# Kernel optimization log

Hardware: AMD Instinct MI355X
Metric: run time of the kernel (lower is better)

## Reference

```python
import jax, jax.numpy as jnp
import numpy as np

B, S, NX, NH = 4, 2048, 1024, 16
HD = NX // NH
MASKED_BIAS = -10000.0


def setup_inputs() -> dict:
    key = jax.random.key(0)
    k1, k2, k3 = jax.random.split(key, 3)
    return {
        "hidden_states": jax.random.normal(k1, (B, S, NX), dtype=jnp.float32),
        "c_attn_w": jax.random.normal(k2, (NX, 3 * NX), dtype=jnp.float32) * 0.02,
        "c_attn_b": jnp.zeros((3 * NX,), dtype=jnp.float32),
        "c_proj_w": jax.random.normal(k3, (NX, NX), dtype=jnp.float32) * 0.02,
        "c_proj_b": jnp.zeros((NX,), dtype=jnp.float32),
    }


def reference(hidden_states, c_attn_w, c_attn_b, c_proj_w, c_proj_b):
    b, s, nx = hidden_states.shape
    # fused QKV projection (Conv1D == x @ W + b)
    qkv = hidden_states @ c_attn_w + c_attn_b          # [b, s, 3*nx]
    q, k, v = jnp.split(qkv, 3, axis=-1)
    # split heads -> [b, h, s, d]
    q = q.reshape(b, s, NH, HD).transpose(0, 2, 1, 3)
    k = k.reshape(b, s, NH, HD).transpose(0, 2, 1, 3)
    v = v.reshape(b, s, NH, HD).transpose(0, 2, 1, 3)
    # scaled scores [b, h, s, s]
    w = jnp.einsum("bhqd,bhkd->bhqk", q, k) / jnp.float32(np.sqrt(HD))
    # causal mask via torch.where(mask, w, -10000.0) semantics
    causal = jnp.tril(jnp.ones((s, s), dtype=bool))
    w = jnp.where(causal[None, None], w, jnp.float32(MASKED_BIAS))
    w = jax.nn.softmax(w, axis=-1)
    a = jnp.einsum("bhqk,bhkd->bhqd", w, v)            # [b, h, s, d]
    # merge heads
    a = a.transpose(0, 2, 1, 3).reshape(b, s, nx)
    # output projection
    return a @ c_proj_w + c_proj_b
```

## Files before the change

kernel.cpp:

```cpp
#include <hip/hip_runtime.h>


typedef __bf16 bf16_t;
typedef __bf16 bf16x8 __attribute__((ext_vector_type(8)));
typedef __bf16 bf16x4 __attribute__((ext_vector_type(4)));
typedef float  f32x4  __attribute__((ext_vector_type(4)));

#define DI __device__ __forceinline__

static constexpr int Bq = 4, Sq = 2048, NXq = 1024, NHq = 16, HDq = 64;

DI void gl2lds16(const void* g, void* l) {
#if defined(__has_builtin)
#if __has_builtin(__builtin_amdgcn_global_load_lds)
  __builtin_amdgcn_global_load_lds(
      (const __attribute__((address_space(1))) void*)g,
      (__attribute__((address_space(3))) void*)l, 16, 0, 0);
  return;
#endif
#endif
  *(bf16x8*)l = *(const bf16x8*)g;
}

DI float fast_exp2(float x) {
#if defined(__has_builtin)
#if __has_builtin(__builtin_amdgcn_exp2f)
  return __builtin_amdgcn_exp2f(x);
#else
  return exp2f(x);
#endif
#else
  return exp2f(x);
#endif
}

__global__ __launch_bounds__(256) void prep(
    const float* __restrict__ X, const float* __restrict__ W1,
    const float* __restrict__ W2, bf16_t* __restrict__ Xb,
    bf16_t* __restrict__ Wt1, bf16_t* __restrict__ Wt2) {
  __shared__ float t[32][33];
  const int id = blockIdx.x, tid = threadIdx.x;
  if (id < 2048) {
    const float* src = X + (size_t)id * 4096;
    bf16_t* dst = Xb + (size_t)id * 4096;
#pragma unroll
    for (int i = 0; i < 4; ++i) {
      float4 v = *(const float4*)(src + i * 1024 + tid * 4);
      bf16x4 o;
      o[0] = (bf16_t)v.x; o[1] = (bf16_t)v.y; o[2] = (bf16_t)v.z; o[3] = (bf16_t)v.w;
      *(bf16x4*)(dst + i * 1024 + tid * 4) = o;
    }
    return;
  }
  const float* in; bf16_t* out; int R, C, bx, by;
  if (id < 5120) {
    int tI = id - 2048; R = 1024; C = 3072; in = W1; out = Wt1;
    bx = (tI % 96) * 32; by = (tI / 96) * 32;
  } else {
    int tI = id - 5120; R = 1024; C = 1024; in = W2; out = Wt2;
    bx = (tI % 32) * 32; by = (tI / 32) * 32;
  }
  int tx = tid & 31, ty = tid >> 5;
#pragma unroll
  for (int i = 0; i < 32; i += 8)
    t[ty + i][tx] = in[(size_t)(by + ty + i) * C + bx + tx];
  __syncthreads();
#pragma unroll
  for (int i = 0; i < 32; i += 8)
    out[(size_t)(bx + ty + i) * R + by + tx] = (bf16_t)t[tx][ty + i];
}

DI void gemm_main(const bf16_t* __restrict__ A, const bf16_t* __restrict__ Bt,
                  int K, f32x4 acc[4][4], bf16_t* As, bf16_t* Bs,
                  int lane, int w) {
  const int wy = w >> 1, wx = w & 1;
  const int l15 = lane & 15, quad = lane >> 4;
  for (int kt = 0; kt < K; kt += 32) {
    __syncthreads();
#pragma unroll
    for (int i = 0; i < 2; ++i) {
      int g = w * 2 + i;
      int row = g * 16 + (lane >> 2);
      int ko = kt + (lane & 3) * 8;
      gl2lds16(A + (size_t)row * K + ko, As + g * 512 + lane * 8);
      gl2lds16(Bt + (size_t)row * K + ko, Bs + g * 512 + lane * 8);
    }
    __syncthreads();
    bf16x8 af[4], bfr[4];
#pragma unroll
    for (int mi = 0; mi < 4; ++mi)
      af[mi] = *(const bf16x8*)(As + (wy * 64 + mi * 16 + l15) * 32 + quad * 8);
#pragma unroll
    for (int ni = 0; ni < 4; ++ni)
      bfr[ni] = *(const bf16x8*)(Bs + (wx * 64 + ni * 16 + l15) * 32 + quad * 8);
#pragma unroll
    for (int mi = 0; mi < 4; ++mi)
#pragma unroll
      for (int ni = 0; ni < 4; ++ni)
        acc[mi][ni] = __builtin_amdgcn_mfma_f32_16x16x32_bf16(
            af[mi], bfr[ni], acc[mi][ni], 0, 0, 0);
  }
}

__global__ __launch_bounds__(256) void gemm_qkv(
    const bf16_t* __restrict__ X, const bf16_t* __restrict__ Wt,
    const float* __restrict__ bias, bf16_t* __restrict__ qw,
    bf16_t* __restrict__ kw, bf16_t* __restrict__ vtw) {
  __shared__ __align__(16) bf16_t As[128 * 32];
  __shared__ __align__(16) bf16_t Bs[128 * 32];
  const int tid = threadIdx.x, lane = tid & 63, w = tid >> 6;
  const int m0 = blockIdx.x * 128, n0 = blockIdx.y * 128;
  f32x4 acc[4][4];
#pragma unroll
  for (int mi = 0; mi < 4; ++mi)
#pragma unroll
    for (int ni = 0; ni < 4; ++ni) acc[mi][ni] = (f32x4){0.f, 0.f, 0.f, 0.f};
  gemm_main(X + (size_t)m0 * NXq, Wt + (size_t)n0 * NXq, NXq, acc, As, Bs, lane, w);

  const int wy = w >> 1, wx = w & 1, l15 = lane & 15, quad = lane >> 4;
  const float qscale = 0.125f * 1.44269504088896340736f;
#pragma unroll
  for (int mi = 0; mi < 4; ++mi) {
    int rowb = m0 + wy * 64 + mi * 16 + quad * 4;
    int bb = rowb >> 11, sl = rowb & 2047;
#pragma unroll
    for (int ni = 0; ni < 4; ++ni) {
      int col = n0 + wx * 64 + ni * 16 + l15;
      float bv = bias[col];
      f32x4 v = acc[mi][ni];
      int sec = col >> 10;
      int c = col & 1023;
      int h = c >> 6, d = c & 63;
      if (sec == 0) {
#pragma unroll
        for (int r = 0; r < 4; ++r)
          qw[(((size_t)bb * NHq + h) * Sq + sl + r) * HDq + d] =
              (bf16_t)((v[r] + bv) * qscale);
      } else if (sec == 1) {
#pragma unroll
        for (int r = 0; r < 4; ++r)
          kw[(((size_t)bb * NHq + h) * Sq + sl + r) * HDq + d] = (bf16_t)(v[r] + bv);
      } else {
        bf16x4 t;
#pragma unroll
        for (int r = 0; r < 4; ++r) t[r] = (bf16_t)(v[r] + bv);
        *(bf16x4*)(vtw + (((size_t)bb * NHq + h) * HDq + d) * Sq + sl) = t;
      }
    }
  }
}

__global__ __launch_bounds__(256, 4) void attn_fwd(
    const bf16_t* __restrict__ qw, const bf16_t* __restrict__ kw,
    const bf16_t* __restrict__ vtw, bf16_t* __restrict__ aw) {
  __shared__ __align__(16) bf16_t Ks[4096], Vs[4096];
  __shared__ __align__(16) bf16_t Ps[4][32 * 72];
  const int tid = threadIdx.x, lane = tid & 63, w = tid >> 6;
  const int l15 = lane & 15, quad = lane >> 4;

  const int id = blockIdx.x;
  const int bh = ((id & 7) << 3) | ((id >> 3) & 7);
  const int k4 = (id >> 6) & 3, quarter = id >> 8;
  int qtile;
  if (quarter == 0)      qtile = 15 - k4;
  else if (quarter == 1) qtile = 8 + k4;
  else if (quarter == 2) qtile = 7 - k4;
  else                   qtile = k4;
  const int b = bh >> 4, h = bh & 15;

  const bf16_t* Qg = qw + ((size_t)bh * Sq + qtile * 128) * HDq;
  const bf16_t* Kg = kw + (size_t)bh * Sq * HDq;
  const bf16_t* Vg = vtw + (size_t)bh * HDq * Sq;

  bf16x8 qf[2][2];
#pragma unroll
  for (int mi = 0; mi < 2; ++mi)
#pragma unroll
    for (int ks = 0; ks < 2; ++ks)
      qf[mi][ks] = *(const bf16x8*)(
          Qg + (size_t)((w * 2 + mi) * 16 + l15) * HDq + ks * 32 + quad * 8);

  f32x4 o[2][4];
  float lsum[2][4];
#pragma unroll
  for (int mi = 0; mi < 2; ++mi) {
#pragma unroll
    for (int dt = 0; dt < 4; ++dt) o[mi][dt] = (f32x4){0.f, 0.f, 0.f, 0.f};
#pragma unroll
    for (int r = 0; r < 4; ++r) lsum[mi][r] = 0.f;
  }

  bf16_t* Pw = &Ps[w][0];
  const int jmax = 2 * qtile + 2;
  for (int jt = 0; jt < jmax; ++jt) {
    __syncthreads();
#pragma unroll
    for (int i = 0; i < 2; ++i) {
      int u = w * 2 + i, p = u >> 2, g = u & 3;
      gl2lds16(Kg + (size_t)(jt * 64 + g * 16 + (lane >> 2)) * HDq + p * 32 + (lane & 3) * 8,
               Ks + u * 512 + lane * 8);
      gl2lds16(Vg + (size_t)(g * 16 + (lane >> 2)) * Sq + jt * 64 + p * 32 + (lane & 3) * 8,
               Vs + u * 512 + lane * 8);
    }
    __syncthreads();

    f32x4 sc[2][4];
#pragma unroll
    for (int mi = 0; mi < 2; ++mi)
#pragma unroll
      for (int nt = 0; nt < 4; ++nt) sc[mi][nt] = (f32x4){0.f, 0.f, 0.f, 0.f};
#pragma unroll
    for (int ks = 0; ks < 2; ++ks)
#pragma unroll
      for (int nt = 0; nt < 4; ++nt) {
        bf16x8 kf = *(const bf16x8*)(Ks + ks * 2048 + nt * 512 + (l15 * 4 + quad) * 8);
        sc[0][nt] = __builtin_amdgcn_mfma_f32_16x16x32_bf16(qf[0][ks], kf, sc[0][nt], 0, 0, 0);
        sc[1][nt] = __builtin_amdgcn_mfma_f32_16x16x32_bf16(qf[1][ks], kf, sc[1][nt], 0, 0, 0);
      }

    if (jt >= 2 * qtile) {
#pragma unroll
      for (int mi = 0; mi < 2; ++mi) {
        int qrow = qtile * 128 + (w * 2 + mi) * 16 + quad * 4;
#pragma unroll
        for (int nt = 0; nt < 4; ++nt) {
          int key = jt * 64 + nt * 16 + l15;
#pragma unroll
          for (int r = 0; r < 4; ++r)
            if (key > qrow + r) sc[mi][nt][r] = -1e30f;
        }
      }
    }

#pragma unroll
    for (int mi = 0; mi < 2; ++mi)
#pragma unroll
      for (int nt = 0; nt < 4; ++nt)
#pragma unroll
        for (int r = 0; r < 4; ++r) {
          float p = fast_exp2(sc[mi][nt][r]);
          lsum[mi][r] += p;
          Pw[(mi * 16 + quad * 4 + r) * 72 + nt * 16 + l15] = (bf16_t)p;
        }

#pragma unroll
    for (int kk = 0; kk < 2; ++kk) {
      bf16x8 ap0 = *(const bf16x8*)(Pw + (size_t)l15 * 72 + kk * 32 + quad * 8);
      bf16x8 ap1 = *(const bf16x8*)(Pw + (size_t)(16 + l15) * 72 + kk * 32 + quad * 8);
#pragma unroll
      for (int dt = 0; dt < 4; ++dt) {
        bf16x8 bv = *(const bf16x8*)(Vs + kk * 2048 + dt * 512 + (l15 * 4 + quad) * 8);
        o[0][dt] = __builtin_amdgcn_mfma_f32_16x16x32_bf16(ap0, bv, o[0][dt], 0, 0, 0);
        o[1][dt] = __builtin_amdgcn_mfma_f32_16x16x32_bf16(ap1, bv, o[1][dt], 0, 0, 0);
      }
    }
  }

  float linv[2][4];
#pragma unroll
  for (int mi = 0; mi < 2; ++mi)
#pragma unroll
    for (int r = 0; r < 4; ++r) {
      float s = lsum[mi][r];
#pragma unroll
      for (int off = 8; off > 0; off >>= 1) s += __shfl_xor(s, off);
      linv[mi][r] = 1.f / s;
    }

#pragma unroll
  for (int mi = 0; mi < 2; ++mi) {
    int s0 = qtile * 128 + (w * 2 + mi) * 16 + quad * 4;
#pragma unroll
    for (int dt = 0; dt < 4; ++dt) {
      int col = h * 64 + dt * 16 + l15;
#pragma unroll
      for (int r = 0; r < 4; ++r)
        aw[((size_t)b * Sq + s0 + r) * NXq + col] = (bf16_t)(o[mi][dt][r] * linv[mi][r]);
    }
  }
}

__global__ __launch_bounds__(256) void gemm_proj(
    const bf16_t* __restrict__ Aa, const bf16_t* __restrict__ Wt,
    const float* __restrict__ bias, float* __restrict__ out) {
  __shared__ __align__(16) bf16_t As[128 * 32];
  __shared__ __align__(16) bf16_t Bs[128 * 32];
  const int tid = threadIdx.x, lane = tid & 63, w = tid >> 6;
  const int m0 = blockIdx.x * 128, n0 = blockIdx.y * 128;
  f32x4 acc[4][4];
#pragma unroll
  for (int mi = 0; mi < 4; ++mi)
#pragma unroll
    for (int ni = 0; ni < 4; ++ni) acc[mi][ni] = (f32x4){0.f, 0.f, 0.f, 0.f};
  gemm_main(Aa + (size_t)m0 * NXq, Wt + (size_t)n0 * NXq, NXq, acc, As, Bs, lane, w);

  const int wy = w >> 1, wx = w & 1, l15 = lane & 15, quad = lane >> 4;
#pragma unroll
  for (int mi = 0; mi < 4; ++mi) {
    int rowb = m0 + wy * 64 + mi * 16 + quad * 4;
#pragma unroll
    for (int ni = 0; ni < 4; ++ni) {
      int col = n0 + wx * 64 + ni * 16 + l15;
      float bv = bias[col];
#pragma unroll
      for (int r = 0; r < 4; ++r)
        out[(size_t)(rowb + r) * NXq + col] = acc[mi][ni][r] + bv;
    }
  }
}

extern "C" void kernel_launch(void* const* d_in, const int* in_sizes, int n_in,
                              void* d_out, int out_size, void* d_ws, size_t ws_size,
                              hipStream_t stream) {
  const float* hidden   = (const float*)d_in[0];
  const float* c_attn_w = (const float*)d_in[1];
  const float* c_attn_b = (const float*)d_in[2];
  const float* c_proj_w = (const float*)d_in[3];
  const float* c_proj_b = (const float*)d_in[4];
  float* out = (float*)d_out;

  char* ws = (char*)d_ws;
  const size_t szX   = (size_t)8192 * 1024 * 2;
  const size_t szW1  = (size_t)3072 * 1024 * 2;
  const size_t szW2  = (size_t)1024 * 1024 * 2;
  const size_t szQKV = (size_t)Bq * NHq * Sq * HDq * 2;
  bf16_t* Xb  = (bf16_t*)(ws);
  bf16_t* Wt1 = (bf16_t*)(ws + szX);
  bf16_t* Wt2 = (bf16_t*)(ws + szX + szW1);
  bf16_t* qwp = (bf16_t*)(ws + szX + szW1 + szW2);
  bf16_t* kwp = (bf16_t*)(ws + szX + szW1 + szW2 + szQKV);
  bf16_t* vtp = (bf16_t*)(ws + szX + szW1 + szW2 + 2 * szQKV);
  bf16_t* awp = (bf16_t*)(ws + szX + szW1 + szW2 + 3 * szQKV);
  if (ws_size < szX + szW1 + szW2 + 4 * szQKV) return;

  prep<<<dim3(6144), dim3(256), 0, stream>>>(hidden, c_attn_w, c_proj_w,
                                             Xb, Wt1, Wt2);
  gemm_qkv<<<dim3(64, 24), dim3(256), 0, stream>>>(
      Xb, Wt1, c_attn_b, qwp, kwp, vtp);
  attn_fwd<<<dim3(1024), dim3(256), 0, stream>>>(qwp, kwp, vtp, awp);
  gemm_proj<<<dim3(64, 8), dim3(256), 0, stream>>>(
      awp, Wt2, c_proj_b, out);
}
```

Baseline: 241.3 us.

## Rewrite QKV GEMM with 256x192 tiles, double-buffered swizzled LDS and interleaved loads

After: 251.7 us. 1.04x slower.

```diff
diff --git a/kernel.cpp b/kernel.cpp
--- a/kernel.cpp
+++ b/kernel.cpp
@@ -34,6 +34,8 @@
 #endif
 }
 
+DI int swzb(int X) { return X ^ (((X >> 9) & 1) << 5); }
+
 __global__ __launch_bounds__(256) void prep(
     const float* __restrict__ X, const float* __restrict__ W1,
     const float* __restrict__ W2, bf16_t* __restrict__ Xb,
@@ -70,6 +72,179 @@
     out[(size_t)(bx + ty + i) * R + by + tx] = (bf16_t)t[tx][ty + i];
 }
 
+template <int P>
+DI void qkv_loadA(const char* Ap, int wm, int l15, int quad, bf16x8 (&af)[2][2]) {
+#pragma unroll
+  for (int m2 = 0; m2 < 2; ++m2)
+#pragma unroll
+    for (int ks = 0; ks < 2; ++ks) {
+      int X = (wm * 128 + (P * 2 + m2) * 16 + l15) * 128 + ks * 64 + quad * 16;
+      af[m2][ks] = *(const bf16x8*)(Ap + swzb(X));
+    }
+}
+
+template <int P>
+DI void qkv_mfma(const bf16x8 (&af)[2][2], const bf16x8 (&bfr)[3][2],
+                 f32x4 (&acc)[8][3]) {
+  __builtin_amdgcn_s_setprio(1);
+#pragma unroll
+  for (int m2 = 0; m2 < 2; ++m2)
+#pragma unroll
+    for (int ni = 0; ni < 3; ++ni)
+#pragma unroll
+      for (int ks = 0; ks < 2; ++ks)
+        acc[P * 2 + m2][ni] = __builtin_amdgcn_mfma_f32_16x16x32_bf16(
+            af[m2][ks], bfr[ni][ks], acc[P * 2 + m2][ni], 0, 0, 0);
+  __builtin_amdgcn_s_setprio(0);
+}
+
+__global__ __launch_bounds__(512, 2) void gemm_qkv(
+    const bf16_t* __restrict__ Xb, const bf16_t* __restrict__ Wt,
+    const float* __restrict__ bias, bf16_t* __restrict__ qw,
+    bf16_t* __restrict__ kw, bf16_t* __restrict__ vtw) {
+  __shared__ __align__(16) bf16_t AsS[2][256 * 64];
+  __shared__ __align__(16) bf16_t BsS[2][192 * 64];
+  char* AsB = (char*)AsS;
+  char* BsB = (char*)BsS;
+
+  const int tid = threadIdx.x, lane = tid & 63, w = tid >> 6;
+  const int l15 = lane & 15, quad = lane >> 4;
+  const int wm = w >> 2, wn = w & 3;
+
+  const int flat = blockIdx.x;
+  const int sw = (flat & 7) * 64 + (flat >> 3);
+  const int m0 = (sw & 31) * 256, n0 = (sw >> 5) * 192;
+
+  const char* Ag = (const char*)(Xb + (size_t)m0 * NXq);
+  const char* Bg = (const char*)(Wt + (size_t)n0 * NXq);
+
+  int aX[4], bX[3];
+  size_t aoff[4], boff[3];
+#pragma unroll
+  for (int u = 0; u < 4; ++u) {
+    int X = (u * 8 + w) * 1024 + lane * 16;
+    int Y = swzb(X);
+    aX[u] = X;
+    aoff[u] = (size_t)(Y >> 7) * 2048 + (Y & 127);
+  }
+#pragma unroll
+  for (int u = 0; u < 3; ++u) {
+    int X = (u * 8 + w) * 1024 + lane * 16;
+    int Y = swzb(X);
+    bX[u] = X;
+    boff[u] = (size_t)(Y >> 7) * 2048 + (Y & 127);
+  }
+
+  f32x4 acc[8][3];
+#pragma unroll
+  for (int mi = 0; mi < 8; ++mi)
+#pragma unroll
+    for (int ni = 0; ni < 3; ++ni) acc[mi][ni] = (f32x4){0.f, 0.f, 0.f, 0.f};
+
+#pragma unroll
+  for (int u = 0; u < 4; ++u) gl2lds16(Ag + aoff[u], AsB + aX[u]);
+#pragma unroll
+  for (int u = 0; u < 3; ++u) gl2lds16(Bg + boff[u], BsB + bX[u]);
+#pragma unroll
+  for (int u = 0; u < 3; ++u) gl2lds16(Bg + 128 + boff[u], BsB + 24576 + bX[u]);
+  asm volatile("s_waitcnt vmcnt(3)" ::: "memory");
+  __builtin_amdgcn_s_barrier();
+
+  const int NT = NXq / 64;
+#pragma unroll 1
+  for (int t = 0; t < NT; ++t) {
+    const char* Ap = AsB + (t & 1) * 32768;
+    const char* Bp = BsB + (t & 1) * 24576;
+    char* Aq = AsB + ((t + 1) & 1) * 32768;
+    char* Bn = BsB + (t & 1) * 24576;
+    const char* gAn = Ag + (size_t)(t + 1) * 128;
+    const char* gBn = Bg + (size_t)(t + 2) * 128;
+    const bool sA = (t + 1) < NT, sB = (t + 2) < NT;
+
+    bf16x8 bfr[3][2], af[2][2];
+
+#pragma unroll
+    for (int ni = 0; ni < 3; ++ni)
+#pragma unroll
+      for (int ks = 0; ks < 2; ++ks) {
+        int X = (wn * 48 + ni * 16 + l15) * 128 + ks * 64 + quad * 16;
+        bfr[ni][ks] = *(const bf16x8*)(Bp + swzb(X));
+      }
+    qkv_loadA<0>(Ap, wm, l15, quad, af);
+    if (sA) {
+      gl2lds16(gAn + aoff[0], Aq + aX[0]);
+      gl2lds16(gAn + aoff[1], Aq + aX[1]);
+    }
+    __builtin_amdgcn_s_barrier();
+    asm volatile("s_waitcnt lgkmcnt(0)");
+    qkv_mfma<0>(af, bfr, acc);
+    __builtin_amdgcn_s_barrier();
+
+    qkv_loadA<1>(Ap, wm, l15, quad, af);
+    if (sA) {
+      gl2lds16(gAn + aoff[2], Aq + aX[2]);
+      gl2lds16(gAn + aoff[3], Aq + aX[3]);
+    }
+    __builtin_amdgcn_s_barrier();
+    asm volatile("s_waitcnt lgkmcnt(0)");
+    qkv_mfma<1>(af, bfr, acc);
+    __builtin_amdgcn_s_barrier();
+
+    qkv_loadA<2>(Ap, wm, l15, quad, af);
+    if (sB) {
+      gl2lds16(gBn + boff[0], Bn + bX[0]);
+      gl2lds16(gBn + boff[1], Bn + bX[1]);
+    }
+    __builtin_amdgcn_s_barrier();
+    asm volatile("s_waitcnt lgkmcnt(0)");
+    qkv_mfma<2>(af, bfr, acc);
+    __builtin_amdgcn_s_barrier();
+
+    qkv_loadA<3>(Ap, wm, l15, quad, af);
+    if (sB) gl2lds16(gBn + boff[2], Bn + bX[2]);
+    __builtin_amdgcn_s_barrier();
+    asm volatile("s_waitcnt lgkmcnt(0)");
+    qkv_mfma<3>(af, bfr, acc);
+    if (sB) {
+      asm volatile("s_waitcnt vmcnt(3)" ::: "memory");
+    } else if (sA) {
+      asm volatile("s_waitcnt vmcnt(0)" ::: "memory");
+    }
+    __builtin_amdgcn_s_barrier();
+  }
+
+  const float qscale = 0.125f * 1.44269504088896340736f;
+#pragma unroll
+  for (int mi = 0; mi < 8; ++mi) {
+    int rowb = m0 + wm * 128 + mi * 16 + quad * 4;
+    int bb = rowb >> 11, sl = rowb & 2047;
+#pragma unroll
+    for (int ni = 0; ni < 3; ++ni) {
+      int col = n0 + wn * 48 + ni * 16 + l15;
+      float bv = bias[col];
+      f32x4 v = acc[mi][ni];
+      int sec = col >> 10;
+      int c = col & 1023;
+      int h = c >> 6, d = c & 63;
+      if (sec == 0) {
+#pragma unroll
+        for (int r = 0; r < 4; ++r)
+          qw[(((size_t)bb * NHq + h) * Sq + sl + r) * HDq + d] =
+              (bf16_t)((v[r] + bv) * qscale);
+      } else if (sec == 1) {
+#pragma unroll
+        for (int r = 0; r < 4; ++r)
+          kw[(((size_t)bb * NHq + h) * Sq + sl + r) * HDq + d] = (bf16_t)(v[r] + bv);
+      } else {
+        bf16x4 tv;
+#pragma unroll
+        for (int r = 0; r < 4; ++r) tv[r] = (bf16_t)(v[r] + bv);
+        *(bf16x4*)(vtw + (((size_t)bb * NHq + h) * HDq + d) * Sq + sl) = tv;
+      }
+    }
+  }
+}
+
 DI void gemm_main(const bf16_t* __restrict__ A, const bf16_t* __restrict__ Bt,
                   int K, f32x4 acc[4][4], bf16_t* As, bf16_t* Bs,
                   int lane, int w) {
@@ -99,54 +274,6 @@
       for (int ni = 0; ni < 4; ++ni)
         acc[mi][ni] = __builtin_amdgcn_mfma_f32_16x16x32_bf16(
             af[mi], bfr[ni], acc[mi][ni], 0, 0, 0);
-  }
-}
-
-__global__ __launch_bounds__(256) void gemm_qkv(
-    const bf16_t* __restrict__ X, const bf16_t* __restrict__ Wt,
-    const float* __restrict__ bias, bf16_t* __restrict__ qw,
-    bf16_t* __restrict__ kw, bf16_t* __restrict__ vtw) {
-  __shared__ __align__(16) bf16_t As[128 * 32];
-  __shared__ __align__(16) bf16_t Bs[128 * 32];
-  const int tid = threadIdx.x, lane = tid & 63, w = tid >> 6;
-  const int m0 = blockIdx.x * 128, n0 = blockIdx.y * 128;
-  f32x4 acc[4][4];
-#pragma unroll
-  for (int mi = 0; mi < 4; ++mi)
-#pragma unroll
-    for (int ni = 0; ni < 4; ++ni) acc[mi][ni] = (f32x4){0.f, 0.f, 0.f, 0.f};
-  gemm_main(X + (size_t)m0 * NXq, Wt + (size_t)n0 * NXq, NXq, acc, As, Bs, lane, w);
-
-  const int wy = w >> 1, wx = w & 1, l15 = lane & 15, quad = lane >> 4;
-  const float qscale = 0.125f * 1.44269504088896340736f;
-#pragma unroll
-  for (int mi = 0; mi < 4; ++mi) {
-    int rowb = m0 + wy * 64 + mi * 16 + quad * 4;
-    int bb = rowb >> 11, sl = rowb & 2047;
-#pragma unroll
-    for (int ni = 0; ni < 4; ++ni) {
-      int col = n0 + wx * 64 + ni * 16 + l15;
-      float bv = bias[col];
-      f32x4 v = acc[mi][ni];
-      int sec = col >> 10;
-      int c = col & 1023;
-      int h = c >> 6, d = c & 63;
-      if (sec == 0) {
-#pragma unroll
-        for (int r = 0; r < 4; ++r)
-          qw[(((size_t)bb * NHq + h) * Sq + sl + r) * HDq + d] =
-              (bf16_t)((v[r] + bv) * qscale);
-      } else if (sec == 1) {
-#pragma unroll
-        for (int r = 0; r < 4; ++r)
-          kw[(((size_t)bb * NHq + h) * Sq + sl + r) * HDq + d] = (bf16_t)(v[r] + bv);
-      } else {
-        bf16x4 t;
-#pragma unroll
-        for (int r = 0; r < 4; ++r) t[r] = (bf16_t)(v[r] + bv);
-        *(bf16x4*)(vtw + (((size_t)bb * NHq + h) * HDq + d) * Sq + sl) = t;
-      }
-    }
   }
 }
 
@@ -335,7 +462,7 @@
 
   prep<<<dim3(6144), dim3(256), 0, stream>>>(hidden, c_attn_w, c_proj_w,
                                              Xb, Wt1, Wt2);
-  gemm_qkv<<<dim3(64, 24), dim3(256), 0, stream>>>(
+  gemm_qkv<<<dim3(512), dim3(512), 0, stream>>>(
       Xb, Wt1, c_attn_b, qwp, kwp, vtp);
   attn_fwd<<<dim3(1024), dim3(256), 0, stream>>>(qwp, kwp, vtp, awp);
   gemm_proj<<<dim3(64, 8), dim3(256), 0, stream>>>(
```

## Double-buffer K/V tiles and keep P in registers via transposed QK MFMA

Applied to the files above, without the earlier changes.

After: 232.7 us (median of 4 runs). -3.6%, faster.

```diff
diff --git a/kernel.cpp b/kernel.cpp
--- a/kernel.cpp
+++ b/kernel.cpp
@@ -5,6 +5,8 @@
 typedef __bf16 bf16x8 __attribute__((ext_vector_type(8)));
 typedef __bf16 bf16x4 __attribute__((ext_vector_type(4)));
 typedef float  f32x4  __attribute__((ext_vector_type(4)));
+typedef unsigned int u32;
+typedef unsigned int u32x4 __attribute__((ext_vector_type(4)));
 
 #define DI __device__ __forceinline__
 
@@ -34,6 +36,12 @@
 #endif
 }
 
+DI u32 pk_bf16(float lo, float hi) {
+  u32 r;
+  asm("v_cvt_pk_bf16_f32 %0, %1, %2" : "=v"(r) : "v"(lo), "v"(hi));
+  return r;
+}
+
 __global__ __launch_bounds__(256) void prep(
     const float* __restrict__ X, const float* __restrict__ W1,
     const float* __restrict__ W2, bf16_t* __restrict__ Xb,
@@ -153,10 +161,10 @@
 __global__ __launch_bounds__(256, 4) void attn_fwd(
     const bf16_t* __restrict__ qw, const bf16_t* __restrict__ kw,
     const bf16_t* __restrict__ vtw, bf16_t* __restrict__ aw) {
-  __shared__ __align__(16) bf16_t Ks[4096], Vs[4096];
-  __shared__ __align__(16) bf16_t Ps[4][32 * 72];
+  __shared__ __align__(16) bf16_t Ks[2][4096], Vs[2][4096];
   const int tid = threadIdx.x, lane = tid & 63, w = tid >> 6;
   const int l15 = lane & 15, quad = lane >> 4;
+  const int q2b = quad >> 1;
 
   const int id = blockIdx.x;
   const int bh = ((id & 7) << 3) | ((id >> 3) & 7);
@@ -181,91 +189,129 @@
           Qg + (size_t)((w * 2 + mi) * 16 + l15) * HDq + ks * 32 + quad * 8);
 
   f32x4 o[2][4];
-  float lsum[2][4];
-#pragma unroll
-  for (int mi = 0; mi < 2; ++mi) {
+  float ls[2] = {0.f, 0.f};
+#pragma unroll
+  for (int mi = 0; mi < 2; ++mi)
 #pragma unroll
     for (int dt = 0; dt < 4; ++dt) o[mi][dt] = (f32x4){0.f, 0.f, 0.f, 0.f};
-#pragma unroll
-    for (int r = 0; r < 4; ++r) lsum[mi][r] = 0.f;
-  }
-
-  bf16_t* Pw = &Ps[w][0];
+
+  const int u0 = w * 2, u1 = w * 2 + 1;
+  const int p0 = u0 >> 2, g0 = u0 & 3, p1 = u1 >> 2, g1 = u1 & 3;
+  const int rin = lane >> 2;
+  const int sig = (rin & 3) | ((rin & 4) << 1) | ((rin & 8) >> 1);
+  const size_t kOff0 = (size_t)(g0 * 16 + sig) * HDq + p0 * 32 + (lane & 3) * 8;
+  const size_t kOff1 = (size_t)(g1 * 16 + sig) * HDq + p1 * 32 + (lane & 3) * 8;
+  const size_t vRow0 = (size_t)(g0 * 16 + rin) * Sq + p0 * 32 + (lane & 3) * 8;
+  const size_t vRow1 = (size_t)(g1 * 16 + rin) * Sq + p1 * 32 + (lane & 3) * 8;
+
   const int jmax = 2 * qtile + 2;
+
+  gl2lds16(Kg + kOff0,  &Ks[0][u0 * 512 + lane * 8]);
+  gl2lds16(Vg + vRow0,  &Vs[0][u0 * 512 + lane * 8]);
+  gl2lds16(Kg + kOff1,  &Ks[0][u1 * 512 + lane * 8]);
+  gl2lds16(Vg + vRow1,  &Vs[0][u1 * 512 + lane * 8]);
+
   for (int jt = 0; jt < jmax; ++jt) {
-    __syncthreads();
-#pragma unroll
-    for (int i = 0; i < 2; ++i) {
-      int u = w * 2 + i, p = u >> 2, g = u & 3;
-      gl2lds16(Kg + (size_t)(jt * 64 + g * 16 + (lane >> 2)) * HDq + p * 32 + (lane & 3) * 8,
-               Ks + u * 512 + lane * 8);
-      gl2lds16(Vg + (size_t)(g * 16 + (lane >> 2)) * Sq + jt * 64 + p * 32 + (lane & 3) * 8,
-               Vs + u * 512 + lane * 8);
-    }
-    __syncthreads();
+    const int cur = jt & 1;
+    asm volatile("s_waitcnt vmcnt(0)" ::: "memory");
+    __builtin_amdgcn_s_barrier();
+    if (jt + 1 < jmax) {
+      const int nb = cur ^ 1;
+      gl2lds16(Kg + (size_t)(jt + 1) * 64 * HDq + kOff0, &Ks[nb][u0 * 512 + lane * 8]);
+      gl2lds16(Vg + vRow0 + (size_t)(jt + 1) * 64,       &Vs[nb][u0 * 512 + lane * 8]);
+      gl2lds16(Kg + (size_t)(jt + 1) * 64 * HDq + kOff1, &Ks[nb][u1 * 512 + lane * 8]);
+      gl2lds16(Vg + vRow1 + (size_t)(jt + 1) * 64,       &Vs[nb][u1 * 512 + lane * 8]);
+    }
+    const bf16_t* Kc = &Ks[cur][0];
+    const bf16_t* Vc = &Vs[cur][0];
 
     f32x4 sc[2][4];
 #pragma unroll
     for (int mi = 0; mi < 2; ++mi)
 #pragma unroll
       for (int nt = 0; nt < 4; ++nt) sc[mi][nt] = (f32x4){0.f, 0.f, 0.f, 0.f};
+    __builtin_amdgcn_s_setprio(1);
 #pragma unroll
     for (int ks = 0; ks < 2; ++ks)
 #pragma unroll
       for (int nt = 0; nt < 4; ++nt) {
-        bf16x8 kf = *(const bf16x8*)(Ks + ks * 2048 + nt * 512 + (l15 * 4 + quad) * 8);
-        sc[0][nt] = __builtin_amdgcn_mfma_f32_16x16x32_bf16(qf[0][ks], kf, sc[0][nt], 0, 0, 0);
-        sc[1][nt] = __builtin_amdgcn_mfma_f32_16x16x32_bf16(qf[1][ks], kf, sc[1][nt], 0, 0, 0);
-      }
+        bf16x8 kf = *(const bf16x8*)(Kc + ks * 2048 + nt * 512 + (l15 * 4 + quad) * 8);
+        sc[0][nt] = __builtin_amdgcn_mfma_f32_16x16x32_bf16(kf, qf[0][ks], sc[0][nt], 0, 0, 0);
+        sc[1][nt] = __builtin_amdgcn_mfma_f32_16x16x32_bf16(kf, qf[1][ks], sc[1][nt], 0, 0, 0);
+      }
+    __builtin_amdgcn_s_setprio(0);
 
     if (jt >= 2 * qtile) {
+      const int kb = jt * 64 + ((quad & 1) << 3) + (q2b << 2);
 #pragma unroll
       for (int mi = 0; mi < 2; ++mi) {
-        int qrow = qtile * 128 + (w * 2 + mi) * 16 + quad * 4;
-#pragma unroll
-        for (int nt = 0; nt < 4; ++nt) {
-          int key = jt * 64 + nt * 16 + l15;
+        int qrow = qtile * 128 + (w * 2 + mi) * 16 + l15;
+#pragma unroll
+        for (int nt = 0; nt < 4; ++nt)
 #pragma unroll
           for (int r = 0; r < 4; ++r)
-            if (key > qrow + r) sc[mi][nt][r] = -1e30f;
-        }
-      }
-    }
-
-#pragma unroll
-    for (int mi = 0; mi < 2; ++mi)
+            if (kb + nt * 16 + r > qrow) sc[mi][nt][r] = -1e30f;
+      }
+    }
+
+    bf16x8 pa[2][2];
+#pragma unroll
+    for (int mi = 0; mi < 2; ++mi) {
+      float pv[4][4];
 #pragma unroll
       for (int nt = 0; nt < 4; ++nt)
 #pragma unroll
         for (int r = 0; r < 4; ++r) {
           float p = fast_exp2(sc[mi][nt][r]);
-          lsum[mi][r] += p;
-          Pw[(mi * 16 + quad * 4 + r) * 72 + nt * 16 + l15] = (bf16_t)p;
+          pv[nt][r] = p;
+          ls[mi] += p;
         }
-
+      u32 c0[4], c1[4];
+#pragma unroll
+      for (int nt = 0; nt < 4; ++nt) {
+        c0[nt] = pk_bf16(pv[nt][0], pv[nt][1]);
+        c1[nt] = pk_bf16(pv[nt][2], pv[nt][3]);
+      }
+#pragma unroll
+      for (int kk = 0; kk < 2; ++kk) {
+        u32 oc0 = q2b ? c0[2 * kk + 1] : c0[2 * kk];
+        u32 oc1 = q2b ? c1[2 * kk + 1] : c1[2 * kk];
+        u32 sd0 = q2b ? c0[2 * kk] : c0[2 * kk + 1];
+        u32 sd1 = q2b ? c1[2 * kk] : c1[2 * kk + 1];
+        u32 rc0 = (u32)__shfl_xor((int)sd0, 32);
+        u32 rc1 = (u32)__shfl_xor((int)sd1, 32);
+        u32x4 wv;
+        wv[0] = q2b ? rc0 : oc0;
+        wv[1] = q2b ? rc1 : oc1;
+        wv[2] = q2b ? oc0 : rc0;
+        wv[3] = q2b ? oc1 : rc1;
+        pa[mi][kk] = __builtin_bit_cast(bf16x8, wv);
+      }
+    }
+
+    __builtin_amdgcn_s_setprio(1);
 #pragma unroll
     for (int kk = 0; kk < 2; ++kk) {
-      bf16x8 ap0 = *(const bf16x8*)(Pw + (size_t)l15 * 72 + kk * 32 + quad * 8);
-      bf16x8 ap1 = *(const bf16x8*)(Pw + (size_t)(16 + l15) * 72 + kk * 32 + quad * 8);
 #pragma unroll
       for (int dt = 0; dt < 4; ++dt) {
-        bf16x8 bv = *(const bf16x8*)(Vs + kk * 2048 + dt * 512 + (l15 * 4 + quad) * 8);
-        o[0][dt] = __builtin_amdgcn_mfma_f32_16x16x32_bf16(ap0, bv, o[0][dt], 0, 0, 0);
-        o[1][dt] = __builtin_amdgcn_mfma_f32_16x16x32_bf16(ap1, bv, o[1][dt], 0, 0, 0);
-      }
-    }
+        bf16x8 bv = *(const bf16x8*)(Vc + kk * 2048 + dt * 512 + (l15 * 4 + quad) * 8);
+        o[0][dt] = __builtin_amdgcn_mfma_f32_16x16x32_bf16(pa[0][kk], bv, o[0][dt], 0, 0, 0);
+        o[1][dt] = __builtin_amdgcn_mfma_f32_16x16x32_bf16(pa[1][kk], bv, o[1][dt], 0, 0, 0);
+      }
+    }
+    __builtin_amdgcn_s_setprio(0);
   }
 
   float linv[2][4];
 #pragma unroll
-  for (int mi = 0; mi < 2; ++mi)
-#pragma unroll
-    for (int r = 0; r < 4; ++r) {
-      float s = lsum[mi][r];
-#pragma unroll
-      for (int off = 8; off > 0; off >>= 1) s += __shfl_xor(s, off);
-      linv[mi][r] = 1.f / s;
-    }
+  for (int mi = 0; mi < 2; ++mi) {
+    float s = ls[mi];
+    s += __shfl_xor(s, 16);
+    s += __shfl_xor(s, 32);
+#pragma unroll
+    for (int r = 0; r < 4; ++r)
+      linv[mi][r] = 1.f / __shfl(s, quad * 4 + r);
+  }
 
 #pragma unroll
   for (int mi = 0; mi < 2; ++mi) {
```
